# Optimization experiments

Hardware: AMD Instinct MI355X
Metric: run time of the kernel (lower is better)

The kernel has to match this reference:

```python
import jax, jax.numpy as jnp
import numpy as np
from jax import lax

B, H, W, C = 2, 96, 96, 96
D_STATE, D_CONV, EXPAND = 16, 3, 2
D_INNER = EXPAND * C            # 192 (VSSBlock inner width)
DM = D_INNER                    # Mamba d_model; Mamba expand=1 -> mamba d_inner == DM
DT_RANK = -(-DM // 16)          # ceil(192/16) = 12


def setup_inputs() -> dict:
    key = jax.random.key(0)
    ks = jax.random.split(key, 12)
    s = lambda k, shp, sc=0.02: jax.random.normal(k, shp, jnp.float32) * sc
    return {
        "x": jax.random.normal(ks[0], (B, H, W, C), jnp.float32),
        "norm_w": jnp.ones((C,), jnp.float32),
        "norm_b": jnp.zeros((C,), jnp.float32),
        "in_proj_w": s(ks[1], (C, 2 * D_INNER)),
        "conv2d_w": s(ks[2], (D_INNER, 1, D_CONV, D_CONV), 0.1),   # depthwise OIHW
        "m_in_proj_w": s(ks[3], (DM, 2 * DM)),
        "m_conv1d_w": s(ks[4], (DM, 1, D_CONV), 0.1),              # depthwise causal OIL
        "m_conv1d_b": jnp.zeros((DM,), jnp.float32),
        "m_x_proj_w": s(ks[5], (DM, DT_RANK + 2 * D_STATE)),
        "m_dt_proj_w": s(ks[6], (DT_RANK, DM), 0.1),
        "m_dt_proj_b": s(ks[7], (DM,), 0.1),
        "m_A_log": jnp.log(jnp.broadcast_to(
            jnp.arange(1, D_STATE + 1, dtype=jnp.float32), (DM, D_STATE))),
        "m_D": jnp.ones((DM,), jnp.float32),
        "m_out_proj_w": s(ks[8], (DM, DM)),
        "out_proj_w": s(ks[9], (D_INNER, C)),
    }


def _layernorm(x, w, b, eps=1e-5):
    mu = x.mean(-1, keepdims=True)
    var = jnp.mean(jnp.square(x - mu), -1, keepdims=True)
    return (x - mu) * lax.rsqrt(var + eps) * w + b


def _selective_scan(u, delta, A, Bm, Cm, Dv):
    # u, delta: (B,L,D); A: (D,N); Bm, Cm: (B,L,N); Dv: (D,)
    dA = jnp.exp(jnp.einsum('bld,dn->bldn', delta, A))           # (B,L,D,N)
    dBu = jnp.einsum('bld,bln->bldn', delta * u, Bm)             # (B,L,D,N)

    def step(h, inp):
        dA_t, dBu_t, C_t = inp
        h = dA_t * h + dBu_t                                      # (B,D,N)
        y = jnp.einsum('bdn,bn->bd', h, C_t)
        return h, y

    h0 = jnp.zeros((u.shape[0], A.shape[0], A.shape[1]), u.dtype)
    xs = (dA.transpose(1, 0, 2, 3), dBu.transpose(1, 0, 2, 3), Cm.transpose(1, 0, 2))
    _, ys = lax.scan(step, h0, xs)
    return ys.transpose(1, 0, 2) + u * Dv                         # (B,L,D)


def _mamba(seq, m_in_proj_w, m_conv1d_w, m_conv1d_b, m_x_proj_w,
           m_dt_proj_w, m_dt_proj_b, m_A_log, m_D, m_out_proj_w):
    # seq: (B,L,DM)
    xm, z = jnp.split(seq @ m_in_proj_w, 2, axis=-1)
    # causal depthwise conv1d over L
    xc = lax.conv_general_dilated(
        jnp.transpose(xm, (0, 2, 1)), m_conv1d_w, (1,), [(D_CONV - 1, 0)],
        feature_group_count=DM, dimension_numbers=('NCH', 'OIH', 'NCH'))
    xm = jax.nn.silu(jnp.transpose(xc + m_conv1d_b[None, :, None], (0, 2, 1)))
    x_dbl = xm @ m_x_proj_w
    dt, Bm, Cm = jnp.split(x_dbl, [DT_RANK, DT_RANK + D_STATE], axis=-1)
    delta = jax.nn.softplus(dt @ m_dt_proj_w + m_dt_proj_b)
    A = -jnp.exp(m_A_log)
    y = _selective_scan(xm, delta, A, Bm, Cm, m_D)
    return (y * jax.nn.silu(z)) @ m_out_proj_w


def reference(x, norm_w, norm_b, in_proj_w, conv2d_w, m_in_proj_w, m_conv1d_w,
              m_conv1d_b, m_x_proj_w, m_dt_proj_w, m_dt_proj_b, m_A_log, m_D,
              m_out_proj_w, out_proj_w):
    Bsz, Hh, Ww, _ = x.shape
    xn = _layernorm(x, norm_w, norm_b)
    x_in, x_gate = jnp.split(xn @ in_proj_w, 2, axis=-1)          # (B,H,W,D_INNER) x2
    # depthwise 3x3 conv, 'same' padding
    xc = lax.conv_general_dilated(
        jnp.transpose(x_in, (0, 3, 1, 2)), conv2d_w, (1, 1), [(1, 1), (1, 1)],
        feature_group_count=D_INNER, dimension_numbers=('NCHW', 'OIHW', 'NCHW'))
    xc = jax.nn.silu(jnp.transpose(xc, (0, 2, 3, 1)))
    seq = xc.reshape(Bsz, Hh * Ww, D_INNER)
    y = _mamba(seq, m_in_proj_w, m_conv1d_w, m_conv1d_b, m_x_proj_w,
               m_dt_proj_w, m_dt_proj_b, m_A_log, m_D, m_out_proj_w)
    y = y.reshape(Bsz, Hh, Ww, D_INNER) * jax.nn.silu(x_gate)
    return x + y @ out_proj_w
```

## Files before the change

### kernel.cpp

```cpp
#include <hip/hip_runtime.h>

#define DEV_INLINE __device__ __forceinline__

constexpr int BATCH = 2;
constexpr int HH = 96, WW = 96, CC = 96;
constexpr int DI = 192;
constexpr int NS = 16;
constexpr int LSEQ = HH * WW;
constexpr int TT = BATCH * LSEQ;
constexpr int CHUNK = 16;
constexpr int NCHUNK = LSEQ / CHUNK;
constexpr int SUP = 24, NSUP = NCHUNK / SUP;
constexpr int QDN = DI * NS;

typedef __attribute__((ext_vector_type(8))) short bf16x8;
typedef __attribute__((ext_vector_type(4))) float f32x4;

DEV_INLINE float silu_f(float x) { return x / (1.f + __expf(-x)); }
DEV_INLINE float softplus_f(float x) {
  return fmaxf(x, 0.f) + log1pf(__expf(-fabsf(x)));
}
DEV_INLINE ushort f2bf(float f) {
  union { float f; unsigned u; } c; c.f = f;
  unsigned u = c.u + 0x7FFF + ((c.u >> 16) & 1);
  return (ushort)(u >> 16);
}
DEV_INLINE float bf2f(ushort u) {
  union { unsigned u; float f; } c; c.u = ((unsigned)u) << 16; return c.f;
}

__global__ __launch_bounds__(256)
void castw_kernel(const float* __restrict__ w0, const float* __restrict__ w1,
                  const float* __restrict__ w2, const float* __restrict__ w3,
                  const float* __restrict__ wx, const float* __restrict__ wdt,
                  const float* __restrict__ wc1,
                  ushort* __restrict__ t0, ushort* __restrict__ t1,
                  ushort* __restrict__ t2, ushort* __restrict__ t3,
                  ushort* __restrict__ t4, ushort* __restrict__ t5,
                  float* __restrict__ cwT)
{
  int id = blockIdx.x * 256 + threadIdx.x;
  if (id < 36864) {
    int k = id / 384, n = id % 384;
    t0[n * 96 + k] = f2bf(w0[id]);
  } else if (id < 110592) {
    int j = id - 36864; int k = j / 384, n = j % 384;
    t1[n * 192 + k] = f2bf(w1[j]);
  } else if (id < 147456) {
    int j = id - 110592; int k = j / 192, n = j % 192;
    t2[n * 192 + k] = f2bf(w2[j]);
  } else if (id < 165888) {
    int j = id - 147456; int k = j / 96, n = j % 96;
    t3[n * 192 + k] = f2bf(w3[j]);
  } else if (id < 172032) {
    int j = id - 165888;
    t3[96 * 192 + j] = 0;
  } else if (id < 180480) {
    int j = id - 172032; int k = j / 44, c = j % 44;
    int r = (c < 12) ? (32 + c) : (c < 28 ? (c - 12) : (16 + c - 28));
    t4[r * 192 + k] = f2bf(wx[j]);
  } else if (id < 181248) {
    int j = id - 180480;
    t4[44 * 192 + j] = 0;
  } else if (id < 183552) {
    int j = id - 181248; int r = j / 192, d = j % 192;
    t5[d * 32 + r] = f2bf(wdt[j]);
  } else if (id < 187392) {
    int j = id - 183552; int d = j / 20, r = 12 + j % 20;
    t5[d * 32 + r] = 0;
  } else if (id < 187968) {
    int j = id - 187392; int d = j / 3, k = j % 3;
    cwT[k * 192 + d] = wc1[j];
  }
}

__global__ __launch_bounds__(256)
void ln_inproj_kernel(const float* __restrict__ x, const float* __restrict__ nw,
                      const float* __restrict__ nbias, const ushort* __restrict__ Wt0,
                      ushort* __restrict__ xz0)
{
  __shared__ ushort sA[128][104];
  const int tid = threadIdx.x;
  const int m0 = blockIdx.x * 128;
  const int n0 = blockIdx.y * 64;
  {
    const int tok = tid >> 1, h = tid & 1;
    const float* xr = x + (size_t)(m0 + tok) * 96 + h * 48;
    float v[48];
    float s = 0.f, ss = 0.f;
#pragma unroll
    for (int i = 0; i < 12; ++i) {
      float4 t4 = *(const float4*)(xr + i * 4);
      v[i*4+0] = t4.x; v[i*4+1] = t4.y; v[i*4+2] = t4.z; v[i*4+3] = t4.w;
      s += (t4.x + t4.y) + (t4.z + t4.w);
      ss += (t4.x*t4.x + t4.y*t4.y) + (t4.z*t4.z + t4.w*t4.w);
    }
    s += __shfl_xor(s, 1);
    ss += __shfl_xor(ss, 1);
    float mean = s * (1.f/96.f);
    float var = ss * (1.f/96.f) - mean*mean;
    float rstd = rsqrtf(var + 1e-5f);
    const float* wr = nw + h*48;
    const float* br = nbias + h*48;
#pragma unroll
    for (int i = 0; i < 12; ++i) {
      float4 w4 = *(const float4*)(wr + i*4);
      float4 b4 = *(const float4*)(br + i*4);
      unsigned p0 = (unsigned)f2bf((v[i*4+0]-mean)*rstd*w4.x + b4.x)
                  | ((unsigned)f2bf((v[i*4+1]-mean)*rstd*w4.y + b4.y) << 16);
      unsigned p1 = (unsigned)f2bf((v[i*4+2]-mean)*rstd*w4.z + b4.z)
                  | ((unsigned)f2bf((v[i*4+3]-mean)*rstd*w4.w + b4.w) << 16);
      unsigned* dst = (unsigned*)&sA[tok][h*48 + i*4];
      dst[0] = p0; dst[1] = p1;
    }
  }
  __syncthreads();

  const int wid = tid >> 6, lane = tid & 63;
  const int wm = wid >> 1, wn = wid & 1;
  const int l16 = lane & 15, quad = lane >> 4;
  const f32x4 z4 = {0.f, 0.f, 0.f, 0.f};
  f32x4 acc[4][2];
#pragma unroll
  for (int i = 0; i < 4; ++i)
#pragma unroll
    for (int j = 0; j < 2; ++j) acc[i][j] = z4;

#pragma unroll
  for (int k0 = 0; k0 < 96; k0 += 32) {
    bf16x8 xf[4], wf[2];
#pragma unroll
    for (int i = 0; i < 4; ++i)
      xf[i] = *(const bf16x8*)&sA[wm*64 + i*16 + l16][k0 + quad*8];
#pragma unroll
    for (int j = 0; j < 2; ++j)
      wf[j] = *(const bf16x8*)(Wt0 + (size_t)(n0 + wn*32 + j*16 + l16) * 96 + k0 + quad*8);
#pragma unroll
    for (int i = 0; i < 4; ++i)
#pragma unroll
      for (int j = 0; j < 2; ++j)
        acc[i][j] = __builtin_amdgcn_mfma_f32_16x16x32_bf16(wf[j], xf[i], acc[i][j], 0, 0, 0);
  }
#pragma unroll
  for (int i = 0; i < 4; ++i) {
    const int token = m0 + wm*64 + i*16 + l16;
#pragma unroll
    for (int j = 0; j < 2; ++j) {
      const int nb = n0 + wn*32 + j*16 + quad*4;
      ushort4 o;
      o.x = f2bf(acc[i][j][0]); o.y = f2bf(acc[i][j][1]);
      o.z = f2bf(acc[i][j][2]); o.w = f2bf(acc[i][j][3]);
      *(ushort4*)(xz0 + (size_t)token * 384 + nb) = o;
    }
  }
}

__global__ __launch_bounds__(256)
void conv2d_silu_kernel(const ushort* __restrict__ xz0, const float* __restrict__ w,
                        ushort* __restrict__ xc)
{
  __shared__ float ws[DI * 9];
  for (int i = threadIdx.x; i < DI * 9; i += 256) ws[i] = w[i];
  __syncthreads();
  int id = blockIdx.x * 256 + threadIdx.x;
  int dq = id % 48;
  int p  = id / 48;
  int j = p % WW;
  int i = (p / WW) % HH;
  int b = p / (WW * HH);
  int d = dq * 4;
  float a0 = 0.f, a1 = 0.f, a2 = 0.f, a3 = 0.f;
#pragma unroll
  for (int ki = 0; ki < 3; ++ki) {
    int ii = i + ki - 1;
    if (ii < 0 || ii >= HH) continue;
#pragma unroll
    for (int kj = 0; kj < 3; ++kj) {
      int jj = j + kj - 1;
      if (jj < 0 || jj >= WW) continue;
      const ushort4 v = *(const ushort4*)(xz0 + ((size_t)((b * HH + ii) * WW + jj)) * 384 + d);
      int wk = ki * 3 + kj;
      a0 = fmaf(bf2f(v.x), ws[(d + 0) * 9 + wk], a0);
      a1 = fmaf(bf2f(v.y), ws[(d + 1) * 9 + wk], a1);
      a2 = fmaf(bf2f(v.z), ws[(d + 2) * 9 + wk], a2);
      a3 = fmaf(bf2f(v.w), ws[(d + 3) * 9 + wk], a3);
    }
  }
  ushort4 o;
  o.x = f2bf(silu_f(a0)); o.y = f2bf(silu_f(a1));
  o.z = f2bf(silu_f(a2)); o.w = f2bf(silu_f(a3));
  *(ushort4*)(xc + (size_t)p * DI + d) = o;
}

__global__ __launch_bounds__(256)
void mfma_gemm_kernel(const ushort* __restrict__ A, int lda,
                      const ushort* __restrict__ Bt, int ldb,
                      ushort* __restrict__ Cout, int ldc, int K)
{
  const int tid = threadIdx.x;
  const int wid = tid >> 6, lane = tid & 63;
  const int wm = wid >> 1, wn = wid & 1;
  const int m0 = blockIdx.x * 128 + wm * 64;
  const int n0 = blockIdx.y * 64 + wn * 32;
  const int l16 = lane & 15, quad = lane >> 4;

  f32x4 acc[4][2];
  const f32x4 z4 = {0.f, 0.f, 0.f, 0.f};
#pragma unroll
  for (int i = 0; i < 4; ++i)
#pragma unroll
    for (int j = 0; j < 2; ++j) acc[i][j] = z4;

  for (int k0 = 0; k0 < K; k0 += 32) {
    bf16x8 xf[4], wf[2];
#pragma unroll
    for (int i = 0; i < 4; ++i)
      xf[i] = *(const bf16x8*)(A + (size_t)(m0 + i * 16 + l16) * lda + k0 + quad * 8);
#pragma unroll
    for (int j = 0; j < 2; ++j)
      wf[j] = *(const bf16x8*)(Bt + (size_t)(n0 + j * 16 + l16) * ldb + k0 + quad * 8);
#pragma unroll
    for (int i = 0; i < 4; ++i)
#pragma unroll
      for (int j = 0; j < 2; ++j)
        acc[i][j] = __builtin_amdgcn_mfma_f32_16x16x32_bf16(wf[j], xf[i], acc[i][j], 0, 0, 0);
  }
#pragma unroll
  for (int i = 0; i < 4; ++i) {
    const int token = m0 + i * 16 + l16;
#pragma unroll
    for (int j = 0; j < 2; ++j) {
      const int nb = n0 + j * 16 + quad * 4;
      ushort4 o;
      o.x = f2bf(acc[i][j][0]); o.y = f2bf(acc[i][j][1]);
      o.z = f2bf(acc[i][j][2]); o.w = f2bf(acc[i][j][3]);
      *(ushort4*)(Cout + (size_t)token * ldc + nb) = o;
    }
  }
}

__global__ __launch_bounds__(256)
void conv1d_silu_kernel(const ushort* __restrict__ xz1, const float* __restrict__ cwT,
                        const float* __restrict__ bias, ushort* __restrict__ xm)
{
  int id = blockIdx.x * 256 + threadIdx.x;
  int dq = id % 48;
  int t  = id / 48;
  int l  = t % LSEQ;
  int d  = dq * 4;
  float4 b4 = *(const float4*)(bias + d);
  float a0 = b4.x, a1 = b4.y, a2 = b4.z, a3 = b4.w;
#pragma unroll
  for (int k = 0; k < 3; ++k) {
    if (l + k - 2 < 0) continue;
    const ushort4 v = *(const ushort4*)(xz1 + (size_t)(t + k - 2) * 384 + d);
    const float4 w4 = *(const float4*)(cwT + k * 192 + d);
    a0 = fmaf(bf2f(v.x), w4.x, a0);
    a1 = fmaf(bf2f(v.y), w4.y, a1);
    a2 = fmaf(bf2f(v.z), w4.z, a2);
    a3 = fmaf(bf2f(v.w), w4.w, a3);
  }
  ushort4 o;
  o.x = f2bf(silu_f(a0)); o.y = f2bf(silu_f(a1));
  o.z = f2bf(silu_f(a2)); o.w = f2bf(silu_f(a3));
  *(ushort4*)(xm + (size_t)t * DI + d) = o;
}

__global__ __launch_bounds__(256)
void xproj_kernel(const ushort* __restrict__ xmb, const ushort* __restrict__ Wxt,
                  float* __restrict__ xdbl_bc, ushort* __restrict__ dtpad)
{
  const int w = blockIdx.x * 4 + (threadIdx.x >> 6);
  const int lane = threadIdx.x & 63;
  const int s = w / 3, tile = w % 3;
  const int l16 = lane & 15, quad = lane >> 4;
  const int token = s * 16 + l16;

  f32x4 acc = {0.f, 0.f, 0.f, 0.f};
#pragma unroll
  for (int k0 = 0; k0 < 192; k0 += 32) {
    bf16x8 xf = *(const bf16x8*)(xmb + (size_t)token * DI + k0 + quad * 8);
    bf16x8 wf = *(const bf16x8*)(Wxt + (size_t)(tile * 16 + l16) * 192 + k0 + quad * 8);
    acc = __builtin_amdgcn_mfma_f32_16x16x32_bf16(wf, xf, acc, 0, 0, 0);
  }
  if (tile < 2) {
    *(float4*)(xdbl_bc + (size_t)token * 32 + tile * 16 + quad * 4) =
        make_float4(acc[0], acc[1], acc[2], acc[3]);
  } else {
    ushort4 o;
    o.x = f2bf(acc[0]); o.y = f2bf(acc[1]); o.z = f2bf(acc[2]); o.w = f2bf(acc[3]);
    *(ushort4*)(dtpad + (size_t)token * 32 + quad * 4) = o;
    *(ushort4*)(dtpad + (size_t)token * 32 + 16 + quad * 4) = make_ushort4(0, 0, 0, 0);
  }
}

__global__ __launch_bounds__(256)
void dtproj_kernel(const ushort* __restrict__ dtpad, const ushort* __restrict__ Wdtt,
                   const float* __restrict__ bdt, ushort* __restrict__ dlt)
{
  const int w = blockIdx.x * 4 + (threadIdx.x >> 6);
  const int lane = threadIdx.x & 63;
  const int s = w / 3, cg = w % 3;
  const int l16 = lane & 15, quad = lane >> 4;
  const int token = s * 16 + l16;
  const f32x4 z4 = {0.f, 0.f, 0.f, 0.f};

  bf16x8 dtf = *(const bf16x8*)(dtpad + (size_t)token * 32 + quad * 8);
  f32x4 acc[4];
#pragma unroll
  for (int jj = 0; jj < 4; ++jj) {
    bf16x8 wf = *(const bf16x8*)(Wdtt + (size_t)(cg * 64 + jj * 16 + l16) * 32 + quad * 8);
    acc[jj] = __builtin_amdgcn_mfma_f32_16x16x32_bf16(wf, dtf, z4, 0, 0, 0);
  }
#pragma unroll
  for (int jj = 0; jj < 4; ++jj) {
    const int nb = cg * 64 + jj * 16 + quad * 4;
    const float4 b4 = *(const float4*)(bdt + nb);
    ushort4 o;
    o.x = f2bf(softplus_f(acc[jj][0] + b4.x));
    o.y = f2bf(softplus_f(acc[jj][1] + b4.y));
    o.z = f2bf(softplus_f(acc[jj][2] + b4.z));
    o.w = f2bf(softplus_f(acc[jj][3] + b4.w));
    *(ushort4*)(dlt + (size_t)token * DI + nb) = o;
  }
}

__global__ __launch_bounds__(192)
void scan1_kernel(const ushort* __restrict__ dlt, const ushort* __restrict__ xmb,
                  const float* __restrict__ bc, const float* __restrict__ Alog,
                  float* __restrict__ P, float* __restrict__ E)
{
  __shared__ float sB[CHUNK][16];
  const int d = threadIdx.x;
  const int g = blockIdx.x % NCHUNK;
  const int b = blockIdx.x / NCHUNK;
  const int t0 = b * LSEQ + g * CHUNK;
  for (int i = threadIdx.x; i < CHUNK * 16; i += 192) {
    int l = i >> 4, j = i & 15;
    sB[l][j] = bc[(size_t)(t0 + l) * 32 + j];
  }
  float Av[16];
#pragma unroll
  for (int j = 0; j < 16; ++j) Av[j] = -__expf(Alog[d * 16 + j]);
  __syncthreads();
  float e[16];
#pragma unroll
  for (int j = 0; j < 16; ++j) e[j] = 0.f;
  float sdl = 0.f;
#pragma unroll 4
  for (int l = 0; l < CHUNK; ++l) {
    const int t = t0 + l;
    float dl = bf2f(dlt[(size_t)t * DI + d]);
    float u  = bf2f(xmb[(size_t)t * DI + d]);
    float du = dl * u;
    sdl += dl;
#pragma unroll
    for (int j = 0; j < 16; ++j) {
      float a = __expf(dl * Av[j]);
      e[j] = fmaf(a, e[j], du * sB[l][j]);
    }
  }
  size_t base = ((size_t)(b * NCHUNK + g)) * QDN + d;
#pragma unroll
  for (int j = 0; j < 16; ++j) {
    P[base + j * 192] = __expf(Av[j] * sdl);
    E[base + j * 192] = e[j];
  }
}

__global__ __launch_bounds__(256)
void scan2a_kernel(const float* __restrict__ P, const float* __restrict__ E,
                   float* __restrict__ SP, float* __restrict__ SE)
{
  int id = blockIdx.x * 256 + threadIdx.x;
  int q = id % QDN;
  int s = (id / QDN) % NSUP;
  int b = id / (QDN * NSUP);
  float cp = 1.f, ce = 0.f;
#pragma unroll 6
  for (int c = 0; c < SUP; ++c) {
    size_t idx = ((size_t)(b * NCHUNK + s * SUP + c)) * QDN + q;
    float p = P[idx], e = E[idx];
    ce = fmaf(p, ce, e);
    cp *= p;
  }
  SP[id] = cp; SE[id] = ce;
}

__global__ __launch_bounds__(256)
void scan2b_kernel(const float* __restrict__ SP, const float* __restrict__ SE,
                   float* __restrict__ Hsup)
{
  int id = blockIdx.x * 256 + threadIdx.x;
  int q = id % QDN;
  int b = id / QDN;
  float carry = 0.f;
#pragma unroll
  for (int s = 0; s < NSUP; ++s) {
    size_t idx = ((size_t)(b * NSUP + s)) * QDN + q;
    Hsup[idx] = carry;
    carry = fmaf(SP[idx], carry, SE[idx]);
  }
}

__global__ __launch_bounds__(256)
void scan2c_kernel(const float* __restrict__ P, const float* __restrict__ E,
                   const float* __restrict__ Hsup, float* __restrict__ Hin)
{
  int id = blockIdx.x * 256 + threadIdx.x;
  int q = id % QDN;
  int s = (id / QDN) % NSUP;
  int b = id / (QDN * NSUP);
  float h = Hsup[id];
#pragma unroll 6
  for (int c = 0; c < SUP; ++c) {
    size_t idx = ((size_t)(b * NCHUNK + s * SUP + c)) * QDN + q;
    Hin[idx] = h;
    h = fmaf(P[idx], h, E[idx]);
  }
}

__global__ __launch_bounds__(192)
void scan3_kernel(const ushort* __restrict__ dlt, const ushort* __restrict__ xmb,
                  const float* __restrict__ bc, const float* __restrict__ Alog,
                  const float* __restrict__ Dv, const ushort* __restrict__ xz1,
                  const float* __restrict__ Hin, ushort* __restrict__ yout)
{
  __shared__ float sBC[CHUNK][32];
  const int d = threadIdx.x;
  const int g = blockIdx.x % NCHUNK;
  const int b = blockIdx.x / NCHUNK;
  const int t0 = b * LSEQ + g * CHUNK;
  for (int i = threadIdx.x; i < CHUNK * 32; i += 192) {
    int l = i >> 5, j = i & 31;
    sBC[l][j] = bc[(size_t)(t0 + l) * 32 + j];
  }
  float Av[16];
#pragma unroll
  for (int j = 0; j < 16; ++j) Av[j] = -__expf(Alog[d * 16 + j]);
  const float Dd = Dv[d];
  float h[16];
  {
    size_t hb = ((size_t)(b * NCHUNK + g)) * QDN + d;
#pragma unroll
    for (int j = 0; j < 16; ++j) h[j] = Hin[hb + j * 192];
  }
  __syncthreads();
#pragma unroll 4
  for (int l = 0; l < CHUNK; ++l) {
    const int t = t0 + l;
    float dl = bf2f(dlt[(size_t)t * DI + d]);
    float u  = bf2f(xmb[(size_t)t * DI + d]);
    float z  = bf2f(xz1[(size_t)t * 384 + 192 + d]);
    float du = dl * u;
    float y0 = 0.f, y1 = 0.f, y2 = 0.f, y3 = 0.f;
#pragma unroll
    for (int j = 0; j < 16; ++j) {
      float a = __expf(dl * Av[j]);
      h[j] = fmaf(a, h[j], du * sBC[l][j]);
      float hc = h[j] * sBC[l][16 + j];
      if ((j & 3) == 0) y0 += hc;
      else if ((j & 3) == 1) y1 += hc;
      else if ((j & 3) == 2) y2 += hc;
      else y3 += hc;
    }
    float y = (y0 + y1) + (y2 + y3) + u * Dd;
    yout[(size_t)t * DI + d] = f2bf(y * silu_f(z));
  }
}

__global__ __launch_bounds__(256)
void outproj_kernel(const ushort* __restrict__ yfin, const ushort* __restrict__ Wt2,
                    const ushort* __restrict__ xz0, const ushort* __restrict__ Wt3,
                    const float* __restrict__ x, float* __restrict__ out)
{
  __shared__ ushort yg_s[32][204];
  const int tid = threadIdx.x;
  const int wid = tid >> 6, lane = tid & 63;
  const int wm = wid >> 1, wn = wid & 1;
  const int l16 = lane & 15, quad = lane >> 4;
  const int m0 = blockIdx.x * 32;
  const f32x4 z4 = {0.f, 0.f, 0.f, 0.f};

  f32x4 acc[6];
#pragma unroll
  for (int j = 0; j < 6; ++j) acc[j] = z4;
  const int mt = m0 + wm * 16 + l16;
#pragma unroll
  for (int k0 = 0; k0 < 192; k0 += 32) {
    bf16x8 af = *(const bf16x8*)(yfin + (size_t)mt * 192 + k0 + quad * 8);
#pragma unroll
    for (int nj = 0; nj < 6; ++nj) {
      bf16x8 wf = *(const bf16x8*)(Wt2 + (size_t)(wn * 96 + nj * 16 + l16) * 192 + k0 + quad * 8);
      acc[nj] = __builtin_amdgcn_mfma_f32_16x16x32_bf16(wf, af, acc[nj], 0, 0, 0);
    }
  }
#pragma unroll
  for (int nj = 0; nj < 6; ++nj) {
    const int tok = wm * 16 + l16;
    const int nb = wn * 96 + nj * 16 + quad * 4;
    const ushort4 g4 = *(const ushort4*)(xz0 + (size_t)(m0 + tok) * 384 + 192 + nb);
    float v0 = acc[nj][0] * silu_f(bf2f(g4.x));
    float v1 = acc[nj][1] * silu_f(bf2f(g4.y));
    float v2 = acc[nj][2] * silu_f(bf2f(g4.z));
    float v3 = acc[nj][3] * silu_f(bf2f(g4.w));
    unsigned p0 = (unsigned)f2bf(v0) | ((unsigned)f2bf(v1) << 16);
    unsigned p1 = (unsigned)f2bf(v2) | ((unsigned)f2bf(v3) << 16);
    unsigned* dst = (unsigned*)&yg_s[tok][nb];
    dst[0] = p0; dst[1] = p1;
  }
  __syncthreads();

  f32x4 acc2[3];
#pragma unroll
  for (int j = 0; j < 3; ++j) acc2[j] = z4;
#pragma unroll
  for (int k0 = 0; k0 < 192; k0 += 32) {
    bf16x8 af = *(const bf16x8*)&yg_s[wm * 16 + l16][k0 + quad * 8];
#pragma unroll
    for (int nj = 0; nj < 3; ++nj) {
      bf16x8 wf = *(const bf16x8*)(Wt3 + (size_t)(wn * 48 + nj * 16 + l16) * 192 + k0 + quad * 8);
      acc2[nj] = __builtin_amdgcn_mfma_f32_16x16x32_bf16(wf, af, acc2[nj], 0, 0, 0);
    }
  }
#pragma unroll
  for (int nj = 0; nj < 3; ++nj) {
    const int tok = wm * 16 + l16;
    const int nb = wn * 48 + nj * 16 + quad * 4;
    const float4 r4 = *(const float4*)(x + (size_t)(m0 + tok) * 96 + nb);
    *(float4*)(out + (size_t)(m0 + tok) * 96 + nb) =
        make_float4(acc2[nj][0] + r4.x, acc2[nj][1] + r4.y,
                    acc2[nj][2] + r4.z, acc2[nj][3] + r4.w);
  }
}

extern "C" void kernel_launch(void* const* d_in, const int* in_sizes, int n_in,
                              void* d_out, int out_size, void* d_ws, size_t ws_size,
                              hipStream_t stream)
{
  const float* x         = (const float*)d_in[0];
  const float* norm_w    = (const float*)d_in[1];
  const float* norm_b    = (const float*)d_in[2];
  const float* in_proj_w = (const float*)d_in[3];
  const float* conv2d_w  = (const float*)d_in[4];
  const float* m_in_proj = (const float*)d_in[5];
  const float* m_c1d_w   = (const float*)d_in[6];
  const float* m_c1d_b   = (const float*)d_in[7];
  const float* m_x_proj  = (const float*)d_in[8];
  const float* m_dt_w    = (const float*)d_in[9];
  const float* m_dt_b    = (const float*)d_in[10];
  const float* m_A_log   = (const float*)d_in[11];
  const float* m_D       = (const float*)d_in[12];
  const float* m_out_w   = (const float*)d_in[13];
  const float* out_w     = (const float*)d_in[14];
  float* out = (float*)d_out;

  char* wp = (char*)d_ws;
  auto alloc = [&](size_t bytes) {
    char* r = wp; wp += (bytes + 255) & ~(size_t)255; return r;
  };
  ushort* Wt0    = (ushort*)alloc(36864 * 2);
  ushort* Wt1    = (ushort*)alloc(73728 * 2);
  ushort* Wt2    = (ushort*)alloc(36864 * 2);
  ushort* Wt3    = (ushort*)alloc(24576 * 2);
  ushort* Wxt    = (ushort*)alloc(9216 * 2);
  ushort* Wdtt   = (ushort*)alloc(6144 * 2);
  float*  cw1T   = (float*)alloc(576 * 4);
  ushort* xz0    = (ushort*)alloc((size_t)TT * 384 * 2);
  ushort* xc_bf  = (ushort*)alloc((size_t)TT * 192 * 2);
  ushort* xz1    = (ushort*)alloc((size_t)TT * 384 * 2);
  ushort* xmb_bf = (ushort*)alloc((size_t)TT * 192 * 2);
  ushort* dtpad  = (ushort*)alloc((size_t)TT * 32 * 2);
  float*  bc     = (float*)alloc((size_t)TT * 32 * 4);
  ushort* dlt    = (ushort*)alloc((size_t)TT * 192 * 2);
  float*  P      = (float*)alloc((size_t)BATCH * NCHUNK * QDN * 4);
  float*  E      = (float*)alloc((size_t)BATCH * NCHUNK * QDN * 4);
  float*  SP     = (float*)alloc((size_t)BATCH * NSUP * QDN * 4);
  float*  SE     = (float*)alloc((size_t)BATCH * NSUP * QDN * 4);
  float*  Hsup   = (float*)alloc((size_t)BATCH * NSUP * QDN * 4);
  float*  Hin    = (float*)alloc((size_t)BATCH * NCHUNK * QDN * 4);
  ushort* yfin   = (ushort*)alloc((size_t)TT * 192 * 2);

  castw_kernel<<<735, 256, 0, stream>>>(in_proj_w, m_in_proj, m_out_w, out_w,
                                        m_x_proj, m_dt_w, m_c1d_w,
                                        Wt0, Wt1, Wt2, Wt3, Wxt, Wdtt, cw1T);
  ln_inproj_kernel<<<dim3(TT / 128, 6), 256, 0, stream>>>(x, norm_w, norm_b, Wt0, xz0);
  conv2d_silu_kernel<<<TT * 48 / 256, 256, 0, stream>>>(xz0, conv2d_w, xc_bf);
  mfma_gemm_kernel<<<dim3(TT / 128, 6), 256, 0, stream>>>(xc_bf, 192, Wt1, 192, xz1, 384, 192);
  conv1d_silu_kernel<<<TT * 48 / 256, 256, 0, stream>>>(xz1, cw1T, m_c1d_b, xmb_bf);
  xproj_kernel<<<TT / 16 * 3 / 4, 256, 0, stream>>>(xmb_bf, Wxt, bc, dtpad);
  dtproj_kernel<<<TT / 16 * 3 / 4, 256, 0, stream>>>(dtpad, Wdtt, m_dt_b, dlt);
  scan1_kernel<<<BATCH * NCHUNK, 192, 0, stream>>>(dlt, xmb_bf, bc, m_A_log, P, E);
  scan2a_kernel<<<BATCH * NSUP * QDN / 256, 256, 0, stream>>>(P, E, SP, SE);
  scan2b_kernel<<<BATCH * QDN / 256, 256, 0, stream>>>(SP, SE, Hsup);
  scan2c_kernel<<<BATCH * NSUP * QDN / 256, 256, 0, stream>>>(P, E, Hsup, Hin);
  scan3_kernel<<<BATCH * NCHUNK, 192, 0, stream>>>(dlt, xmb_bf, bc, m_A_log, m_D, xz1, Hin, yfin);
  outproj_kernel<<<TT / 32, 256, 0, stream>>>(yfin, Wt2, xz0, Wt3, x, out);
}
```

Measured before the change: 239.5 us.

## Fuse conv1d, x_proj, dt_proj and chunk-scan pass into one kernel; pack P/E as bf16

Four kernels (causal conv1d+silu, x_proj, dt_proj, scan chunk summaries) are merged into one block-per-32-tokens kernel. Intermediates stay in shared memory, so the dtpad buffer and the re-reads of xm, dlt and bc by the scan are gone, along with three launches. The chunk decay/state pairs P and E are packed as bf16 into a single 32-bit word, and Hin is stored in bf16, which halves the traffic for the chunk-carry passes. The cost is lower precision in the carried scan state and a scan-summary stage with only 384 tasks per block, so 128 of the 256 threads sit idle on the second pass.

After: 237.1 us. Within noise of the previous version (-1.0%).

```diff
diff --git a/kernel.cpp b/kernel.cpp
--- a/kernel.cpp
+++ b/kernel.cpp
@@ -240,136 +240,145 @@
 }
 
 __global__ __launch_bounds__(256)
-void conv1d_silu_kernel(const ushort* __restrict__ xz1, const float* __restrict__ cwT,
-                        const float* __restrict__ bias, ushort* __restrict__ xm)
-{
-  int id = blockIdx.x * 256 + threadIdx.x;
-  int dq = id % 48;
-  int t  = id / 48;
-  int l  = t % LSEQ;
-  int d  = dq * 4;
-  float4 b4 = *(const float4*)(bias + d);
-  float a0 = b4.x, a1 = b4.y, a2 = b4.z, a3 = b4.w;
-#pragma unroll
-  for (int k = 0; k < 3; ++k) {
-    if (l + k - 2 < 0) continue;
-    const ushort4 v = *(const ushort4*)(xz1 + (size_t)(t + k - 2) * 384 + d);
-    const float4 w4 = *(const float4*)(cwT + k * 192 + d);
-    a0 = fmaf(bf2f(v.x), w4.x, a0);
-    a1 = fmaf(bf2f(v.y), w4.y, a1);
-    a2 = fmaf(bf2f(v.z), w4.z, a2);
-    a3 = fmaf(bf2f(v.w), w4.w, a3);
-  }
-  ushort4 o;
-  o.x = f2bf(silu_f(a0)); o.y = f2bf(silu_f(a1));
-  o.z = f2bf(silu_f(a2)); o.w = f2bf(silu_f(a3));
-  *(ushort4*)(xm + (size_t)t * DI + d) = o;
-}
-
-__global__ __launch_bounds__(256)
-void xproj_kernel(const ushort* __restrict__ xmb, const ushort* __restrict__ Wxt,
-                  float* __restrict__ xdbl_bc, ushort* __restrict__ dtpad)
-{
-  const int w = blockIdx.x * 4 + (threadIdx.x >> 6);
-  const int lane = threadIdx.x & 63;
-  const int s = w / 3, tile = w % 3;
-  const int l16 = lane & 15, quad = lane >> 4;
-  const int token = s * 16 + l16;
-
-  f32x4 acc = {0.f, 0.f, 0.f, 0.f};
-#pragma unroll
-  for (int k0 = 0; k0 < 192; k0 += 32) {
-    bf16x8 xf = *(const bf16x8*)(xmb + (size_t)token * DI + k0 + quad * 8);
-    bf16x8 wf = *(const bf16x8*)(Wxt + (size_t)(tile * 16 + l16) * 192 + k0 + quad * 8);
-    acc = __builtin_amdgcn_mfma_f32_16x16x32_bf16(wf, xf, acc, 0, 0, 0);
-  }
-  if (tile < 2) {
-    *(float4*)(xdbl_bc + (size_t)token * 32 + tile * 16 + quad * 4) =
-        make_float4(acc[0], acc[1], acc[2], acc[3]);
-  } else {
+void mprep_kernel(const ushort* __restrict__ xz1, const float* __restrict__ cwT,
+                  const float* __restrict__ cb, const ushort* __restrict__ Wxt,
+                  const ushort* __restrict__ Wdtt, const float* __restrict__ bdt,
+                  const float* __restrict__ Alog,
+                  ushort* __restrict__ xmb, ushort* __restrict__ dlt,
+                  float* __restrict__ bc, unsigned* __restrict__ PE)
+{
+  __shared__ ushort sxm[32][204];
+  __shared__ ushort sdlt[32][204];
+  __shared__ float sbc[32][36];
+  const int tid = threadIdx.x;
+  const int bid = blockIdx.x;
+  const int T0 = bid * 32;
+  const f32x4 z4 = {0.f, 0.f, 0.f, 0.f};
+
+  for (int task = tid; task < 1536; task += 256) {
+    int dq = task % 48, tok = task / 48;
+    int t = T0 + tok, l = t % LSEQ;
+    int d = dq * 4;
+    float4 b4 = *(const float4*)(cb + d);
+    float a0 = b4.x, a1 = b4.y, a2 = b4.z, a3 = b4.w;
+#pragma unroll
+    for (int k = 0; k < 3; ++k) {
+      if (l + k - 2 < 0) continue;
+      const ushort4 v = *(const ushort4*)(xz1 + (size_t)(t + k - 2) * 384 + d);
+      const float4 w4 = *(const float4*)(cwT + k * 192 + d);
+      a0 = fmaf(bf2f(v.x), w4.x, a0);
+      a1 = fmaf(bf2f(v.y), w4.y, a1);
+      a2 = fmaf(bf2f(v.z), w4.z, a2);
+      a3 = fmaf(bf2f(v.w), w4.w, a3);
+    }
     ushort4 o;
-    o.x = f2bf(acc[0]); o.y = f2bf(acc[1]); o.z = f2bf(acc[2]); o.w = f2bf(acc[3]);
-    *(ushort4*)(dtpad + (size_t)token * 32 + quad * 4) = o;
-    *(ushort4*)(dtpad + (size_t)token * 32 + 16 + quad * 4) = make_ushort4(0, 0, 0, 0);
-  }
-}
-
-__global__ __launch_bounds__(256)
-void dtproj_kernel(const ushort* __restrict__ dtpad, const ushort* __restrict__ Wdtt,
-                   const float* __restrict__ bdt, ushort* __restrict__ dlt)
-{
-  const int w = blockIdx.x * 4 + (threadIdx.x >> 6);
-  const int lane = threadIdx.x & 63;
-  const int s = w / 3, cg = w % 3;
-  const int l16 = lane & 15, quad = lane >> 4;
-  const int token = s * 16 + l16;
-  const f32x4 z4 = {0.f, 0.f, 0.f, 0.f};
-
-  bf16x8 dtf = *(const bf16x8*)(dtpad + (size_t)token * 32 + quad * 8);
-  f32x4 acc[4];
-#pragma unroll
-  for (int jj = 0; jj < 4; ++jj) {
-    bf16x8 wf = *(const bf16x8*)(Wdtt + (size_t)(cg * 64 + jj * 16 + l16) * 32 + quad * 8);
-    acc[jj] = __builtin_amdgcn_mfma_f32_16x16x32_bf16(wf, dtf, z4, 0, 0, 0);
-  }
-#pragma unroll
-  for (int jj = 0; jj < 4; ++jj) {
-    const int nb = cg * 64 + jj * 16 + quad * 4;
-    const float4 b4 = *(const float4*)(bdt + nb);
-    ushort4 o;
-    o.x = f2bf(softplus_f(acc[jj][0] + b4.x));
-    o.y = f2bf(softplus_f(acc[jj][1] + b4.y));
-    o.z = f2bf(softplus_f(acc[jj][2] + b4.z));
-    o.w = f2bf(softplus_f(acc[jj][3] + b4.w));
-    *(ushort4*)(dlt + (size_t)token * DI + nb) = o;
-  }
-}
-
-__global__ __launch_bounds__(192)
-void scan1_kernel(const ushort* __restrict__ dlt, const ushort* __restrict__ xmb,
-                  const float* __restrict__ bc, const float* __restrict__ Alog,
-                  float* __restrict__ P, float* __restrict__ E)
-{
-  __shared__ float sB[CHUNK][16];
-  const int d = threadIdx.x;
-  const int g = blockIdx.x % NCHUNK;
-  const int b = blockIdx.x / NCHUNK;
-  const int t0 = b * LSEQ + g * CHUNK;
-  for (int i = threadIdx.x; i < CHUNK * 16; i += 192) {
-    int l = i >> 4, j = i & 15;
-    sB[l][j] = bc[(size_t)(t0 + l) * 32 + j];
-  }
-  float Av[16];
-#pragma unroll
-  for (int j = 0; j < 16; ++j) Av[j] = -__expf(Alog[d * 16 + j]);
+    o.x = f2bf(silu_f(a0)); o.y = f2bf(silu_f(a1));
+    o.z = f2bf(silu_f(a2)); o.w = f2bf(silu_f(a3));
+    *(ushort4*)&sxm[tok][d] = o;
+    *(ushort4*)(xmb + (size_t)t * DI + d) = o;
+  }
   __syncthreads();
-  float e[16];
-#pragma unroll
-  for (int j = 0; j < 16; ++j) e[j] = 0.f;
-  float sdl = 0.f;
-#pragma unroll 4
-  for (int l = 0; l < CHUNK; ++l) {
-    const int t = t0 + l;
-    float dl = bf2f(dlt[(size_t)t * DI + d]);
-    float u  = bf2f(xmb[(size_t)t * DI + d]);
-    float du = dl * u;
-    sdl += dl;
+
+  {
+    const int wv = tid >> 6, lane = tid & 63;
+    const int l16 = lane & 15, quad = lane >> 4;
+    const int s = wv & 1, role = wv >> 1;
+    const int tokb = s * 16;
+    if (role == 0) {
+      f32x4 aB = z4, aC = z4;
+#pragma unroll
+      for (int k0 = 0; k0 < 192; k0 += 32) {
+        bf16x8 uf = *(const bf16x8*)&sxm[tokb + l16][k0 + quad * 8];
+        bf16x8 wB = *(const bf16x8*)(Wxt + (size_t)(l16) * 192 + k0 + quad * 8);
+        bf16x8 wC = *(const bf16x8*)(Wxt + (size_t)(16 + l16) * 192 + k0 + quad * 8);
+        aB = __builtin_amdgcn_mfma_f32_16x16x32_bf16(wB, uf, aB, 0, 0, 0);
+        aC = __builtin_amdgcn_mfma_f32_16x16x32_bf16(wC, uf, aC, 0, 0, 0);
+      }
+      float4 vB = make_float4(aB[0], aB[1], aB[2], aB[3]);
+      float4 vC = make_float4(aC[0], aC[1], aC[2], aC[3]);
+      *(float4*)&sbc[tokb + l16][quad * 4] = vB;
+      *(float4*)&sbc[tokb + l16][16 + quad * 4] = vC;
+      *(float4*)(bc + (size_t)(T0 + tokb + l16) * 32 + quad * 4) = vB;
+      *(float4*)(bc + (size_t)(T0 + tokb + l16) * 32 + 16 + quad * 4) = vC;
+    } else {
+      f32x4 aD = z4;
+#pragma unroll
+      for (int k0 = 0; k0 < 192; k0 += 32) {
+        bf16x8 uf = *(const bf16x8*)&sxm[tokb + l16][k0 + quad * 8];
+        bf16x8 wD = *(const bf16x8*)(Wxt + (size_t)(32 + l16) * 192 + k0 + quad * 8);
+        aD = __builtin_amdgcn_mfma_f32_16x16x32_bf16(wD, uf, aD, 0, 0, 0);
+      }
+      bf16x8 dtf;
+#pragma unroll
+      for (int j = 0; j < 8; ++j) {
+        int n = quad * 8 + j;
+        int src = ((n >> 2) & 3) * 16 + l16;
+        float tv = __shfl(aD[j & 3], src);
+        dtf[j] = (short)((n < 16) ? f2bf(tv) : (ushort)0);
+      }
+      f32x4 a2[12];
+#pragma unroll
+      for (int jj = 0; jj < 12; ++jj) {
+        bf16x8 wf = *(const bf16x8*)(Wdtt + (size_t)(jj * 16 + l16) * 32 + quad * 8);
+        a2[jj] = __builtin_amdgcn_mfma_f32_16x16x32_bf16(wf, dtf, z4, 0, 0, 0);
+      }
+#pragma unroll
+      for (int jj = 0; jj < 12; ++jj) {
+        const int nb = jj * 16 + quad * 4;
+        const float4 b4 = *(const float4*)(bdt + nb);
+        ushort4 o;
+        o.x = f2bf(softplus_f(a2[jj][0] + b4.x));
+        o.y = f2bf(softplus_f(a2[jj][1] + b4.y));
+        o.z = f2bf(softplus_f(a2[jj][2] + b4.z));
+        o.w = f2bf(softplus_f(a2[jj][3] + b4.w));
+        *(ushort4*)&sdlt[tokb + l16][nb] = o;
+        *(ushort4*)(dlt + (size_t)(T0 + tokb + l16) * DI + nb) = o;
+      }
+    }
+  }
+  __syncthreads();
+
+  for (int task = tid; task < 384; task += 256) {
+    const int d = task % 192, c = task / 192;
+    float Av[16];
+#pragma unroll
+    for (int j = 0; j < 16; ++j) Av[j] = -__expf(Alog[d * 16 + j]);
+    float e[16];
+#pragma unroll
+    for (int j = 0; j < 16; ++j) e[j] = 0.f;
+    float sdl = 0.f;
+    for (int l = 0; l < CHUNK; ++l) {
+      const int tl = c * 16 + l;
+      float dl = bf2f(sdlt[tl][d]);
+      float u  = bf2f(sxm[tl][d]);
+      const float4 B0 = *(const float4*)&sbc[tl][0];
+      const float4 B1 = *(const float4*)&sbc[tl][4];
+      const float4 B2 = *(const float4*)&sbc[tl][8];
+      const float4 B3 = *(const float4*)&sbc[tl][12];
+      const float Bv[16] = {B0.x, B0.y, B0.z, B0.w, B1.x, B1.y, B1.z, B1.w,
+                            B2.x, B2.y, B2.z, B2.w, B3.x, B3.y, B3.z, B3.w};
+      float du = dl * u;
+      sdl += dl;
+#pragma unroll
+      for (int j = 0; j < 16; ++j) {
+        float a = __expf(dl * Av[j]);
+        e[j] = fmaf(a, e[j], du * Bv[j]);
+      }
+    }
+    const int batch = bid / 288;
+    const int gci = (bid % 288) * 2 + c;
+    size_t base = ((size_t)(batch * NCHUNK + gci)) * QDN + d;
 #pragma unroll
     for (int j = 0; j < 16; ++j) {
-      float a = __expf(dl * Av[j]);
-      e[j] = fmaf(a, e[j], du * sB[l][j]);
-    }
-  }
-  size_t base = ((size_t)(b * NCHUNK + g)) * QDN + d;
-#pragma unroll
-  for (int j = 0; j < 16; ++j) {
-    P[base + j * 192] = __expf(Av[j] * sdl);
-    E[base + j * 192] = e[j];
-  }
-}
-
-__global__ __launch_bounds__(256)
-void scan2a_kernel(const float* __restrict__ P, const float* __restrict__ E,
+      unsigned p = f2bf(__expf(Av[j] * sdl));
+      unsigned ev = f2bf(e[j]);
+      PE[base + j * 192] = (p << 16) | ev;
+    }
+  }
+}
+
+__global__ __launch_bounds__(256)
+void scan2a_kernel(const unsigned* __restrict__ PE,
                    float* __restrict__ SP, float* __restrict__ SE)
 {
   int id = blockIdx.x * 256 + threadIdx.x;
@@ -379,8 +388,9 @@
   float cp = 1.f, ce = 0.f;
 #pragma unroll 6
   for (int c = 0; c < SUP; ++c) {
-    size_t idx = ((size_t)(b * NCHUNK + s * SUP + c)) * QDN + q;
-    float p = P[idx], e = E[idx];
+    unsigned pe = PE[((size_t)(b * NCHUNK + s * SUP + c)) * QDN + q];
+    float p = bf2f((ushort)(pe >> 16));
+    float e = bf2f((ushort)(pe & 0xFFFF));
     ce = fmaf(p, ce, e);
     cp *= p;
   }
@@ -404,8 +414,8 @@
 }
 
 __global__ __launch_bounds__(256)
-void scan2c_kernel(const float* __restrict__ P, const float* __restrict__ E,
-                   const float* __restrict__ Hsup, float* __restrict__ Hin)
+void scan2c_kernel(const unsigned* __restrict__ PE, const float* __restrict__ Hsup,
+                   ushort* __restrict__ Hin)
 {
   int id = blockIdx.x * 256 + threadIdx.x;
   int q = id % QDN;
@@ -415,8 +425,11 @@
 #pragma unroll 6
   for (int c = 0; c < SUP; ++c) {
     size_t idx = ((size_t)(b * NCHUNK + s * SUP + c)) * QDN + q;
-    Hin[idx] = h;
-    h = fmaf(P[idx], h, E[idx]);
+    Hin[idx] = f2bf(h);
+    unsigned pe = PE[idx];
+    float p = bf2f((ushort)(pe >> 16));
+    float e = bf2f((ushort)(pe & 0xFFFF));
+    h = fmaf(p, h, e);
   }
 }
 
@@ -424,7 +437,7 @@
 void scan3_kernel(const ushort* __restrict__ dlt, const ushort* __restrict__ xmb,
                   const float* __restrict__ bc, const float* __restrict__ Alog,
                   const float* __restrict__ Dv, const ushort* __restrict__ xz1,
-                  const float* __restrict__ Hin, ushort* __restrict__ yout)
+                  const ushort* __restrict__ Hin, ushort* __restrict__ yout)
 {
   __shared__ float sBC[CHUNK][32];
   const int d = threadIdx.x;
@@ -443,7 +456,7 @@
   {
     size_t hb = ((size_t)(b * NCHUNK + g)) * QDN + d;
 #pragma unroll
-    for (int j = 0; j < 16; ++j) h[j] = Hin[hb + j * 192];
+    for (int j = 0; j < 16; ++j) h[j] = bf2f(Hin[hb + j * 192]);
   }
   __syncthreads();
 #pragma unroll 4
@@ -570,15 +583,13 @@
   ushort* xc_bf  = (ushort*)alloc((size_t)TT * 192 * 2);
   ushort* xz1    = (ushort*)alloc((size_t)TT * 384 * 2);
   ushort* xmb_bf = (ushort*)alloc((size_t)TT * 192 * 2);
-  ushort* dtpad  = (ushort*)alloc((size_t)TT * 32 * 2);
   float*  bc     = (float*)alloc((size_t)TT * 32 * 4);
   ushort* dlt    = (ushort*)alloc((size_t)TT * 192 * 2);
-  float*  P      = (float*)alloc((size_t)BATCH * NCHUNK * QDN * 4);
-  float*  E      = (float*)alloc((size_t)BATCH * NCHUNK * QDN * 4);
+  unsigned* PE   = (unsigned*)alloc((size_t)BATCH * NCHUNK * QDN * 4);
   float*  SP     = (float*)alloc((size_t)BATCH * NSUP * QDN * 4);
   float*  SE     = (float*)alloc((size_t)BATCH * NSUP * QDN * 4);
   float*  Hsup   = (float*)alloc((size_t)BATCH * NSUP * QDN * 4);
-  float*  Hin    = (float*)alloc((size_t)BATCH * NCHUNK * QDN * 4);
+  ushort* Hin    = (ushort*)alloc((size_t)BATCH * NCHUNK * QDN * 2);
   ushort* yfin   = (ushort*)alloc((size_t)TT * 192 * 2);
 
   castw_kernel<<<735, 256, 0, stream>>>(in_proj_w, m_in_proj, m_out_w, out_w,
@@ -587,13 +598,11 @@
   ln_inproj_kernel<<<dim3(TT / 128, 6), 256, 0, stream>>>(x, norm_w, norm_b, Wt0, xz0);
   conv2d_silu_kernel<<<TT * 48 / 256, 256, 0, stream>>>(xz0, conv2d_w, xc_bf);
   mfma_gemm_kernel<<<dim3(TT / 128, 6), 256, 0, stream>>>(xc_bf, 192, Wt1, 192, xz1, 384, 192);
-  conv1d_silu_kernel<<<TT * 48 / 256, 256, 0, stream>>>(xz1, cw1T, m_c1d_b, xmb_bf);
-  xproj_kernel<<<TT / 16 * 3 / 4, 256, 0, stream>>>(xmb_bf, Wxt, bc, dtpad);
-  dtproj_kernel<<<TT / 16 * 3 / 4, 256, 0, stream>>>(dtpad, Wdtt, m_dt_b, dlt);
-  scan1_kernel<<<BATCH * NCHUNK, 192, 0, stream>>>(dlt, xmb_bf, bc, m_A_log, P, E);
-  scan2a_kernel<<<BATCH * NSUP * QDN / 256, 256, 0, stream>>>(P, E, SP, SE);
+  mprep_kernel<<<TT / 32, 256, 0, stream>>>(xz1, cw1T, m_c1d_b, Wxt, Wdtt, m_dt_b,
+                                            m_A_log, xmb_bf, dlt, bc, PE);
+  scan2a_kernel<<<BATCH * NSUP * QDN / 256, 256, 0, stream>>>(PE, SP, SE);
   scan2b_kernel<<<BATCH * QDN / 256, 256, 0, stream>>>(SP, SE, Hsup);
-  scan2c_kernel<<<BATCH * NSUP * QDN / 256, 256, 0, stream>>>(P, E, Hsup, Hin);
+  scan2c_kernel<<<BATCH * NSUP * QDN / 256, 256, 0, stream>>>(PE, Hsup, Hin);
   scan3_kernel<<<BATCH * NCHUNK, 192, 0, stream>>>(dlt, xmb_bf, bc, m_A_log, m_D, xz1, Hin, yfin);
   outproj_kernel<<<TT / 32, 256, 0, stream>>>(yfin, Wt2, xz0, Wt3, x, out);
 }
```
